# Kernel tuning notes

Hardware: AMD Instinct MI355X
Metric: run time of the kernel (lower is better)

Reference implementation:

```python
import jax, jax.numpy as jnp
import numpy as np

DIM = 1024
NUM_HEADS = 16
HEAD_DIM = DIM // NUM_HEADS
FF = 4 * DIM
B, T, S = 8, 512, 4096


def setup_inputs() -> dict:
    key = jax.random.key(0)
    ks = jax.random.split(key, 14)
    sc = 1.0 / np.sqrt(DIM)
    inp = {
        "x": jax.random.normal(ks[0], (B, T, DIM), jnp.float32),
        "inp": jax.random.normal(ks[1], (B, S, DIM), jnp.float32),
        # attention projections
        "Wq": jax.random.normal(ks[2], (DIM, DIM), jnp.float32) * sc,
        "bq": jnp.zeros((DIM,), jnp.float32),
        "Wk": jax.random.normal(ks[3], (DIM, DIM), jnp.float32) * sc,
        "bk": jnp.zeros((DIM,), jnp.float32),
        "Wv": jax.random.normal(ks[4], (DIM, DIM), jnp.float32) * sc,
        "bv": jnp.zeros((DIM,), jnp.float32),
        "Wo": jax.random.normal(ks[5], (DIM, DIM), jnp.float32) * sc,
        "bo": jnp.zeros((DIM,), jnp.float32),
        # MLP
        "W1": jax.random.normal(ks[6], (DIM, FF), jnp.float32) * sc,
        "b1": jnp.zeros((FF,), jnp.float32),
        "W2": jax.random.normal(ks[7], (FF, DIM), jnp.float32) * (1.0 / np.sqrt(FF)),
        "b2": jnp.zeros((DIM,), jnp.float32),
    }
    return inp


def _perceiver_layer(x, inp, Wq, bq, Wk, bk, Wv, bv, Wo, bo, W1, b1, W2, b2):
    b, t, _ = x.shape
    s = inp.shape[1]
    q = (x @ Wq + bq).reshape(b, t, NUM_HEADS, HEAD_DIM)
    k = (inp @ Wk + bk).reshape(b, s, NUM_HEADS, HEAD_DIM)
    v = (inp @ Wv + bv).reshape(b, s, NUM_HEADS, HEAD_DIM)
    # [b, h, t, s] score tensor (as in original code)
    attn = jnp.einsum('bthd,bshd->bhts', q, k)
    attn = jax.nn.softmax(attn / jnp.sqrt(jnp.float32(HEAD_DIM)), axis=-1)
    out = jnp.einsum('bhts,bshd->bthd', attn, v).reshape(b, t, DIM)
    attn_out = out @ Wo + bo
    x = x + attn_out
    h = jax.nn.gelu(x @ W1 + b1, approximate=True)  # flax nn.gelu default is tanh approx
    x = x + (h @ W2 + b2)
    return x


def reference(x, inp, Wq, bq, Wk, bk, Wv, bv, Wo, bo, W1, b1, W2, b2):
    return _perceiver_layer(x, inp, Wq, bq, Wk, bk, Wv, bv, Wo, bo, W1, b1, W2, b2)
```

## Files before the change

### kernel.cpp

```cpp
#include <hip/hip_runtime.h>
#include <hip/hip_bf16.h>

#define DIM 1024
#define NHEADS 16
#define HDIM 64
#define FF_ 4096
#define BB 8
#define TT 512
#define SS 4096

typedef __attribute__((ext_vector_type(8))) __bf16 bf16x8;
typedef __attribute__((ext_vector_type(4))) float f32x4;
typedef __attribute__((ext_vector_type(4))) unsigned short us4;

#define SWZ(r, b) ((b) ^ (((r) & 7) << 4))

typedef const __attribute__((address_space(1))) void gvoid_t;
typedef __attribute__((address_space(3))) void lvoid_t;

__device__ __forceinline__ void ldst16(const void* g, void* l) {
  __builtin_amdgcn_global_load_lds((gvoid_t*)g, (lvoid_t*)l, 16, 0, 0);
}

__device__ inline unsigned short f2bf(float f) {
  unsigned u = __float_as_uint(f);
  u += 0x7fff + ((u >> 16) & 1);
  return (unsigned short)(u >> 16);
}

__device__ __forceinline__ unsigned cvt_pk(float lo, float hi) {
  unsigned r;
  asm("v_cvt_pk_bf16_f32 %0, %1, %2" : "=v"(r) : "v"(lo), "v"(hi));
  return r;
}

__global__ void cvt_f32_bf16(const float* __restrict__ in,
                             unsigned short* __restrict__ out, int n4) {
  int i = blockIdx.x * blockDim.x + threadIdx.x;
  int stride = gridDim.x * blockDim.x;
  for (; i < n4; i += stride) {
    float4 v = ((const float4*)in)[i];
    uint2 w = {cvt_pk(v.x, v.y), cvt_pk(v.z, v.w)};
    ((uint2*)out)[i] = w;
  }
}

__global__ void transpose_f32_bf16(const float* __restrict__ in,
                                   unsigned short* __restrict__ out,
                                   int R, int C) {
  __shared__ float tile[32][33];
  int bc = blockIdx.x * 32, br = blockIdx.y * 32;
  int tx = threadIdx.x & 31, ty = threadIdx.x >> 5;
#pragma unroll
  for (int i = 0; i < 32; i += 8)
    tile[ty + i][tx] = in[(size_t)(br + ty + i) * C + bc + tx];
  __syncthreads();
#pragma unroll
  for (int i = 0; i < 32; i += 8)
    out[(size_t)(bc + ty + i) * R + br + tx] = f2bf(tile[tx][ty + i]);
}

__global__ void transpose_v(const unsigned short* __restrict__ in,
                            unsigned short* __restrict__ out) {
  __shared__ unsigned short tile[32][33];
  int b = blockIdx.z;
  const unsigned short* ib = in + (size_t)b * SS * 2048 + 1024;
  unsigned short* ob = out + (size_t)b * DIM * SS;
  int bc = blockIdx.x * 32;
  int br = blockIdx.y * 32;
  int tx = threadIdx.x & 31, ty = threadIdx.x >> 5;
#pragma unroll
  for (int i = 0; i < 32; i += 8)
    tile[ty + i][tx] = ib[(size_t)(br + ty + i) * 2048 + bc + tx];
  __syncthreads();
#pragma unroll
  for (int i = 0; i < 32; i += 8)
    ob[(size_t)(bc + ty + i) * SS + br + tx] = tile[tx][ty + i];
}

template <int EPI>
__global__ __launch_bounds__(256, 3)
void gemm_kernel(const unsigned short* __restrict__ A,
                 const unsigned short* __restrict__ Bt,
                 const float* __restrict__ bias,
                 const float* __restrict__ res,
                 void* __restrict__ Cp,
                 unsigned short* __restrict__ C2,
                 int M, int N, int K) {
  __shared__ char smem[32768];
  char* As = smem;
  char* Bs = smem + 16384;

  const int tid = threadIdx.x;
  const int lane = tid & 63;
  const int wave = tid >> 6;
  const int wm = wave >> 1, wn = wave & 1;

  const int flat = blockIdx.y * gridDim.x + blockIdx.x;
  const int cpx = (gridDim.x * gridDim.y) >> 3;
  const int swz = (flat & 7) * cpx + (flat >> 3);
  const int m0 = (swz / gridDim.x) * 128, n0 = (swz % gridDim.x) * 128;

  f32x4 acc[4][4];
#pragma unroll
  for (int i = 0; i < 4; ++i)
#pragma unroll
    for (int j = 0; j < 4; ++j) acc[i][j] = (f32x4){0.f, 0.f, 0.f, 0.f};

  for (int k0 = 0; k0 < K; k0 += 64) {
    __syncthreads();
#pragma unroll
    for (int i = 0; i < 4; ++i) {
      int ch = (wave * 4 + i) * 64 + lane;
      int r = ch >> 3, c8 = (ch & 7) ^ (r & 7);
      ldst16(A + (size_t)(m0 + r) * K + k0 + c8 * 8, As + (wave * 4 + i) * 1024);
      ldst16(Bt + (size_t)(n0 + r) * K + k0 + c8 * 8, Bs + (wave * 4 + i) * 1024);
    }
    __syncthreads();

#pragma unroll
    for (int kk = 0; kk < 2; ++kk) {
      bf16x8 a[4], b[4];
#pragma unroll
      for (int mi = 0; mi < 4; ++mi) {
        int r = wm * 64 + mi * 16 + (lane & 15);
        a[mi] = *(const bf16x8*)(As + r * 128 + SWZ(r, kk * 64 + (lane >> 4) * 16));
      }
#pragma unroll
      for (int ni = 0; ni < 4; ++ni) {
        int r = wn * 64 + ni * 16 + (lane & 15);
        b[ni] = *(const bf16x8*)(Bs + r * 128 + SWZ(r, kk * 64 + (lane >> 4) * 16));
      }
#pragma unroll
      for (int mi = 0; mi < 4; ++mi)
#pragma unroll
        for (int ni = 0; ni < 4; ++ni)
          acc[mi][ni] = __builtin_amdgcn_mfma_f32_16x16x32_bf16(b[ni], a[mi], acc[mi][ni], 0, 0, 0);
    }
  }

  const int q = lane & 15, g4 = (lane >> 4) * 4;
#pragma unroll
  for (int mi = 0; mi < 4; ++mi) {
    int row = m0 + wm * 64 + mi * 16 + q;
#pragma unroll
    for (int ni = 0; ni < 4; ++ni) {
      int colb = n0 + wn * 64 + ni * 16 + g4;
      float4 bv = *(const float4*)(bias + colb);
      f32x4 v = acc[mi][ni];
      float v0 = v[0] + bv.x, v1 = v[1] + bv.y, v2 = v[2] + bv.z, v3 = v[3] + bv.w;
      if (EPI == 0) {
        uint2 w = {cvt_pk(v0, v1), cvt_pk(v2, v3)};
        *(uint2*)((unsigned short*)Cp + (size_t)row * N + colb) = w;
      } else if (EPI == 1) {
        float o[4] = {v0, v1, v2, v3};
#pragma unroll
        for (int j = 0; j < 4; ++j) {
          float u = 0.7978845608028654f * (o[j] + 0.044715f * o[j] * o[j] * o[j]);
          float e = __expf(2.f * u);
          float th = 1.f - 2.f / (e + 1.f);
          o[j] = 0.5f * o[j] * (1.f + th);
        }
        uint2 w = {cvt_pk(o[0], o[1]), cvt_pk(o[2], o[3])};
        *(uint2*)((unsigned short*)Cp + (size_t)row * N + colb) = w;
      } else {
        float4 r4 = *(const float4*)(res + (size_t)row * N + colb);
        float o0 = v0 + r4.x, o1 = v1 + r4.y, o2 = v2 + r4.z, o3 = v3 + r4.w;
        float4 ov = {o0, o1, o2, o3};
        *(float4*)((float*)Cp + (size_t)row * N + colb) = ov;
        if (EPI == 3) {
          uint2 w = {cvt_pk(o0, o1), cvt_pk(o2, o3)};
          *(uint2*)(C2 + (size_t)row * N + colb) = w;
        }
      }
    }
  }
}

__global__ __launch_bounds__(512, 4)
void attn_kernel3(const unsigned short* __restrict__ Qb,
                  const unsigned short* __restrict__ KVb,
                  const unsigned short* __restrict__ Vt,
                  unsigned short* __restrict__ Ob) {
  __shared__ char smem[65536];

  const int tid = threadIdx.x, lane = tid & 63, wave = tid >> 6;
  const int bid = blockIdx.x;
  const int b = bid & 7, qt = (bid >> 3) & 3, h = bid >> 5;
  const int q0 = qt * 128;
  const int q = lane & 15, g = lane >> 4;

  const int rK = tid >> 3;
  const int cK = (tid & 7) ^ (rK & 7);
  char* const Pw = smem + 49152 + wave * 2048;

  const unsigned short* srcQ = Qb + ((size_t)b * TT + q0) * DIM + h * HDIM;
  const unsigned short* srcK = KVb + (size_t)b * SS * 2048 + h * HDIM;
  const unsigned short* srcV = Vt + ((size_t)b * DIM + h * HDIM) * SS;

  {
    int r = tid >> 3, c = (tid & 7) ^ (r & 7);
    ldst16(srcQ + (size_t)r * DIM + c * 8, smem + tid * 16);
    int ch = tid + 512;
    r = ch >> 3; c = (ch & 7) ^ (r & 7);
    ldst16(srcQ + (size_t)r * DIM + c * 8, smem + ch * 16);
  }
  ldst16(srcK + (size_t)rK * 2048 + cK * 8, smem + 16384 + tid * 16);
  ldst16(srcV + (size_t)rK * SS + cK * 8, smem + 32768 + tid * 16);
  __syncthreads();

  bf16x8 qf[2];
  {
    int r = wave * 16 + q;
    qf[0] = *(const bf16x8*)(smem + r * 128 + SWZ(r, g * 16));
    qf[1] = *(const bf16x8*)(smem + r * 128 + SWZ(r, 64 + g * 16));
  }

  f32x4 acc[4];
#pragma unroll
  for (int dt = 0; dt < 4; ++dt) acc[dt] = (f32x4){0.f, 0.f, 0.f, 0.f};
  float lsum = 0.f;
  const float CSC = 0.125f * 1.4426950408889634f;

  const int NT = SS / 64;
  for (int t = 0; t < NT; ++t) {
    char* Kc = smem + 16384 + (t & 1) * 8192;
    char* Vc = smem + 32768 + (t & 1) * 8192;
    if (t + 1 < NT) {
      char* Kn = smem + 16384 + ((t + 1) & 1) * 8192;
      char* Vn = smem + 32768 + ((t + 1) & 1) * 8192;
      ldst16(srcK + (size_t)((t + 1) * 64 + rK) * 2048 + cK * 8, Kn + tid * 16);
      ldst16(srcV + (size_t)rK * SS + (t + 1) * 64 + cK * 8, Vn + tid * 16);
    }

    f32x4 st[4];
#pragma unroll
    for (int si = 0; si < 4; ++si) st[si] = (f32x4){0.f, 0.f, 0.f, 0.f};
#pragma unroll
    for (int kk = 0; kk < 2; ++kk)
#pragma unroll
      for (int si = 0; si < 4; ++si) {
        int r = si * 16 + q;
        bf16x8 kf = *(const bf16x8*)(Kc + r * 128 + SWZ(r, kk * 64 + g * 16));
        st[si] = __builtin_amdgcn_mfma_f32_16x16x32_bf16(kf, qf[kk], st[si], 0, 0, 0);
      }

    float rs = 0.f;
#pragma unroll
    for (int si = 0; si < 4; ++si) {
      float p0 = __builtin_amdgcn_exp2f(st[si][0] * CSC);
      float p1 = __builtin_amdgcn_exp2f(st[si][1] * CSC);
      float p2 = __builtin_amdgcn_exp2f(st[si][2] * CSC);
      float p3 = __builtin_amdgcn_exp2f(st[si][3] * CSC);
      rs += (p0 + p1) + (p2 + p3);
      uint2 w = {cvt_pk(p0, p1), cvt_pk(p2, p3)};
      *(uint2*)(Pw + q * 128 + SWZ(q, si * 32 + g * 8)) = w;
    }
    lsum += rs;

#pragma unroll
    for (int kk = 0; kk < 2; ++kk) {
      bf16x8 pb = *(const bf16x8*)(Pw + q * 128 + SWZ(q, kk * 64 + g * 16));
#pragma unroll
      for (int dt = 0; dt < 4; ++dt) {
        int r = dt * 16 + q;
        bf16x8 va = *(const bf16x8*)(Vc + r * 128 + SWZ(r, kk * 64 + g * 16));
        acc[dt] = __builtin_amdgcn_mfma_f32_16x16x32_bf16(va, pb, acc[dt], 0, 0, 0);
      }
    }
    __syncthreads();
  }

  lsum += __shfl_xor(lsum, 16);
  lsum += __shfl_xor(lsum, 32);
  float inv = 1.0f / lsum;
#pragma unroll
  for (int dt = 0; dt < 4; ++dt) {
    f32x4 v = acc[dt];
    uint2 w = {cvt_pk(v[0] * inv, v[1] * inv), cvt_pk(v[2] * inv, v[3] * inv)};
    *(uint2*)(Pw + q * 128 + SWZ(q, dt * 32 + g * 8)) = w;
  }
  __builtin_amdgcn_s_waitcnt(0);
  int qr = lane >> 2, cb = (lane & 3) * 32;
  uint4 lo = *(const uint4*)(Pw + qr * 128 + SWZ(qr, cb));
  uint4 hi = *(const uint4*)(Pw + qr * 128 + SWZ(qr, cb + 16));
  size_t ob = ((size_t)b * TT + q0 + wave * 16 + qr) * DIM + h * HDIM + (lane & 3) * 16;
  *(uint4*)(Ob + ob) = lo;
  *(uint4*)(Ob + ob + 8) = hi;
}

extern "C" void kernel_launch(void* const* d_in, const int* in_sizes, int n_in,
                              void* d_out, int out_size, void* d_ws, size_t ws_size,
                              hipStream_t stream) {
  const float* x   = (const float*)d_in[0];
  const float* inp = (const float*)d_in[1];
  const float* Wq  = (const float*)d_in[2];
  const float* bq  = (const float*)d_in[3];
  const float* Wk  = (const float*)d_in[4];
  const float* bk  = (const float*)d_in[5];
  const float* Wv  = (const float*)d_in[6];
  const float* bv  = (const float*)d_in[7];
  const float* Wo  = (const float*)d_in[8];
  const float* bo  = (const float*)d_in[9];
  const float* W1  = (const float*)d_in[10];
  const float* b1  = (const float*)d_in[11];
  const float* W2  = (const float*)d_in[12];
  const float* b2  = (const float*)d_in[13];
  float* out = (float*)d_out;

  char* ws = (char*)d_ws;
  const size_t MB = 1024ull * 1024ull;
  unsigned short* Wqt  = (unsigned short*)(ws + 0 * MB);
  unsigned short* Wkt  = (unsigned short*)(ws + 2 * MB);
  unsigned short* Wvt  = (unsigned short*)(ws + 4 * MB);
  unsigned short* Wkvt = Wkt;
  unsigned short* Wot  = (unsigned short*)(ws + 6 * MB);
  unsigned short* W1t  = (unsigned short*)(ws + 8 * MB);
  unsigned short* W2t  = (unsigned short*)(ws + 16 * MB);
  float*          bkv  = (float*)(ws + 24 * MB);
  unsigned short* Qb   = (unsigned short*)(ws + 25 * MB);
  unsigned short* KVb  = (unsigned short*)(ws + 33 * MB);
  float*          x2   = (float*)(ws + 33 * MB);
  unsigned short* x2b  = (unsigned short*)(ws + 49 * MB);
  unsigned short* hb   = (unsigned short*)(ws + 57 * MB);
  unsigned short* inpb = (unsigned short*)(ws + 161 * MB);
  unsigned short* Vt   = (unsigned short*)(ws + 161 * MB);
  unsigned short* xb   = (unsigned short*)(ws + 225 * MB);
  unsigned short* Obf  = (unsigned short*)d_out;

  hipMemcpyAsync(bkv, bk, 1024 * sizeof(float), hipMemcpyDeviceToDevice, stream);
  hipMemcpyAsync(bkv + 1024, bv, 1024 * sizeof(float), hipMemcpyDeviceToDevice, stream);

  cvt_f32_bf16<<<2048, 256, 0, stream>>>(inp, inpb, BB * SS * DIM / 4);
  cvt_f32_bf16<<<1024, 256, 0, stream>>>(x, xb, BB * TT * DIM / 4);

  transpose_f32_bf16<<<dim3(32, 32), 256, 0, stream>>>(Wq, Wqt, 1024, 1024);
  transpose_f32_bf16<<<dim3(32, 32), 256, 0, stream>>>(Wk, Wkt, 1024, 1024);
  transpose_f32_bf16<<<dim3(32, 32), 256, 0, stream>>>(Wv, Wvt, 1024, 1024);
  transpose_f32_bf16<<<dim3(32, 32), 256, 0, stream>>>(Wo, Wot, 1024, 1024);
  transpose_f32_bf16<<<dim3(128, 32), 256, 0, stream>>>(W1, W1t, 1024, 4096);
  transpose_f32_bf16<<<dim3(32, 128), 256, 0, stream>>>(W2, W2t, 4096, 1024);

  gemm_kernel<0><<<dim3(8, 32), 256, 0, stream>>>(xb, Wqt, bq, nullptr, Qb, nullptr, BB * TT, DIM, DIM);
  gemm_kernel<0><<<dim3(16, 256), 256, 0, stream>>>(inpb, Wkvt, bkv, nullptr, KVb, nullptr, BB * SS, 2048, DIM);

  transpose_v<<<dim3(32, 128, 8), 256, 0, stream>>>(KVb, Vt);

  attn_kernel3<<<dim3(512), 512, 0, stream>>>(Qb, KVb, Vt, Obf);

  gemm_kernel<3><<<dim3(8, 32), 256, 0, stream>>>(Obf, Wot, bo, x, x2, x2b, BB * TT, DIM, DIM);
  gemm_kernel<1><<<dim3(32, 32), 256, 0, stream>>>(x2b, W1t, b1, nullptr, hb, nullptr, BB * TT, FF_, DIM);
  gemm_kernel<2><<<dim3(8, 32), 256, 0, stream>>>(hb, W2t, b2, x2, out, nullptr, BB * TT, DIM, FF_);
}
```

Before: 513.9 us.

## Add 256x256 GEMM kernel, fuse V transpose into KV projection epilogue

Adds a new 512-thread GEMM with 256x256 tiles, a multi-stage global-to-LDS pipeline, and a grouped block-index swizzle. It replaces the K/V projection and the W1 MLP GEMM. The K/V projection epilogue writes K into a separate buffer and writes V already transposed, which removes the standalone transpose_v kernel and its extra pass over memory. The risks are that the transposed V stores are scattered 2-byte writes with poor coalescing, and that 128KB of LDS per block limits occupancy.

```diff
diff --git a/kernel.cpp b/kernel.cpp
--- a/kernel.cpp
+++ b/kernel.cpp
@@ -58,24 +58,6 @@
 #pragma unroll
   for (int i = 0; i < 32; i += 8)
     out[(size_t)(bc + ty + i) * R + br + tx] = f2bf(tile[tx][ty + i]);
-}
-
-__global__ void transpose_v(const unsigned short* __restrict__ in,
-                            unsigned short* __restrict__ out) {
-  __shared__ unsigned short tile[32][33];
-  int b = blockIdx.z;
-  const unsigned short* ib = in + (size_t)b * SS * 2048 + 1024;
-  unsigned short* ob = out + (size_t)b * DIM * SS;
-  int bc = blockIdx.x * 32;
-  int br = blockIdx.y * 32;
-  int tx = threadIdx.x & 31, ty = threadIdx.x >> 5;
-#pragma unroll
-  for (int i = 0; i < 32; i += 8)
-    tile[ty + i][tx] = ib[(size_t)(br + ty + i) * 2048 + bc + tx];
-  __syncthreads();
-#pragma unroll
-  for (int i = 0; i < 32; i += 8)
-    ob[(size_t)(bc + ty + i) * SS + br + tx] = tile[tx][ty + i];
 }
 
 template <int EPI>
@@ -177,9 +159,149 @@
   }
 }
 
+template <int EPI>
+__global__ __launch_bounds__(512, 2)
+void gemm256(const unsigned short* __restrict__ A,
+             const unsigned short* __restrict__ Bt,
+             const float* __restrict__ bias,
+             void* __restrict__ Cp,
+             unsigned short* __restrict__ C2,
+             int M, int N, int K) {
+  __shared__ char smem[131072];
+
+  const int tid = threadIdx.x, lane = tid & 63, wave = tid >> 6;
+  const int q = lane & 15, g = lane >> 4;
+  const int wm = wave >> 2, wn = wave & 3;
+
+  const int flat = blockIdx.y * gridDim.x + blockIdx.x;
+  const int cpx = (gridDim.x * gridDim.y) >> 3;
+  const int swz = (flat & 7) * cpx + (flat >> 3);
+  const int m0 = (swz / gridDim.x) * 256, n0 = (swz % gridDim.x) * 256;
+
+  const unsigned short* Arow = A + (size_t)m0 * K;
+  const unsigned short* Brow = Bt + (size_t)n0 * K;
+
+  const int r0 = tid >> 3, c0 = ((tid & 7) ^ (r0 & 7)) * 8;
+  const int r1 = (tid + 512) >> 3, c1 = (((tid + 512) & 7) ^ (r1 & 7)) * 8;
+
+#define STA(buf, half, kt)                                                     \
+  { char* d = smem + (buf) * 32768 + (half) * 16384;                           \
+    const unsigned short* s = Arow + (size_t)((half) * 128) * K + (kt) * 64;   \
+    ldst16(s + (size_t)r0 * K + c0, d + tid * 16);                             \
+    ldst16(s + (size_t)r1 * K + c1, d + 8192 + tid * 16); }
+#define STB(buf, half, kt)                                                     \
+  { char* d = smem + 65536 + (buf) * 32768 + (half) * 16384;                   \
+    const unsigned short* s = Brow + (size_t)((half) * 128) * K + (kt) * 64;   \
+    ldst16(s + (size_t)r0 * K + c0, d + tid * 16);                             \
+    ldst16(s + (size_t)r1 * K + c1, d + 8192 + tid * 16); }
+
+  f32x4 acc[8][4];
+#pragma unroll
+  for (int i = 0; i < 8; ++i)
+#pragma unroll
+    for (int j = 0; j < 4; ++j) acc[i][j] = (f32x4){0.f, 0.f, 0.f, 0.f};
+
+  STA(0, 0, 0); STA(0, 1, 0); STB(0, 0, 0); STB(0, 1, 0);
+  STB(1, 0, 1); STB(1, 1, 1); STA(1, 0, 1);
+  asm volatile("s_waitcnt vmcnt(6)" ::: "memory");
+  __builtin_amdgcn_s_barrier();
+
+  const int NKT = K >> 6;
+  for (int kt = 0; kt < NKT; ++kt) {
+    const int cb = kt & 1, nb = cb ^ 1;
+    const char* Ab = smem + cb * 32768;
+    const char* Bb = smem + 65536 + cb * 32768;
+    bf16x8 bfr[4][2];
+
+#pragma unroll
+    for (int p = 0; p < 4; ++p) {
+      if (p == 0) { if (kt + 1 < NKT) STA(nb, 1, kt + 1); }
+      else if (p == 1) { if (kt + 2 < NKT) STB(cb, 0, kt + 2); }
+      else if (p == 2) { if (kt + 2 < NKT) STB(cb, 1, kt + 2); }
+      else            { if (kt + 2 < NKT) STA(cb, 0, kt + 2); }
+
+      bf16x8 af[2][2];
+#pragma unroll
+      for (int i = 0; i < 2; ++i)
+#pragma unroll
+        for (int kk = 0; kk < 2; ++kk) {
+          int r = wm * 128 + (2 * p + i) * 16 + q;
+          af[i][kk] = *(const bf16x8*)(Ab + r * 128 + SWZ(r, kk * 64 + g * 16));
+        }
+      if (p == 0) {
+#pragma unroll
+        for (int nr = 0; nr < 4; ++nr)
+#pragma unroll
+          for (int kk = 0; kk < 2; ++kk) {
+            int r = wn * 64 + nr * 16 + q;
+            bfr[nr][kk] = *(const bf16x8*)(Bb + r * 128 + SWZ(r, kk * 64 + g * 16));
+          }
+      }
+
+      __builtin_amdgcn_s_barrier();
+      asm volatile("s_waitcnt lgkmcnt(0)" ::: "memory");
+      __builtin_amdgcn_sched_barrier(0);
+      __builtin_amdgcn_s_setprio(1);
+#pragma unroll
+      for (int i = 0; i < 2; ++i)
+#pragma unroll
+        for (int nr = 0; nr < 4; ++nr)
+#pragma unroll
+          for (int kk = 0; kk < 2; ++kk)
+            acc[2 * p + i][nr] = __builtin_amdgcn_mfma_f32_16x16x32_bf16(
+                bfr[nr][kk], af[i][kk], acc[2 * p + i][nr], 0, 0, 0);
+      __builtin_amdgcn_s_setprio(0);
+
+      if (p == 1) asm volatile("s_waitcnt vmcnt(10)" ::: "memory");
+      if (p == 3) asm volatile("s_waitcnt vmcnt(8)" ::: "memory");
+      __builtin_amdgcn_s_barrier();
+    }
+  }
+
+  const int g4 = g * 4;
+#pragma unroll
+  for (int mr = 0; mr < 8; ++mr) {
+    int row = m0 + wm * 128 + mr * 16 + q;
+#pragma unroll
+    for (int nr = 0; nr < 4; ++nr) {
+      int colb = n0 + wn * 64 + nr * 16 + g4;
+      float4 bv = *(const float4*)(bias + colb);
+      f32x4 v = acc[mr][nr];
+      float v0 = v[0] + bv.x, v1 = v[1] + bv.y, v2 = v[2] + bv.z, v3 = v[3] + bv.w;
+      if (EPI == 1) {
+        float o[4] = {v0, v1, v2, v3};
+#pragma unroll
+        for (int j = 0; j < 4; ++j) {
+          float u = 0.7978845608028654f * (o[j] + 0.044715f * o[j] * o[j] * o[j]);
+          float e = __expf(2.f * u);
+          float th = 1.f - 2.f / (e + 1.f);
+          o[j] = 0.5f * o[j] * (1.f + th);
+        }
+        uint2 w = {cvt_pk(o[0], o[1]), cvt_pk(o[2], o[3])};
+        *(uint2*)((unsigned short*)Cp + (size_t)row * N + colb) = w;
+      } else {
+        if (n0 < 1024) {
+          uint2 w = {cvt_pk(v0, v1), cvt_pk(v2, v3)};
+          *(uint2*)((unsigned short*)Cp + (size_t)row * 1024 + colb) = w;
+        } else {
+          int b = row >> 12, s = row & 4095;
+          int d0 = colb - 1024;
+          unsigned short* vt = C2 + ((size_t)b * DIM + d0) * SS + s;
+          vt[0] = f2bf(v0);
+          vt[SS] = f2bf(v1);
+          vt[2 * SS] = f2bf(v2);
+          vt[3 * SS] = f2bf(v3);
+        }
+      }
+    }
+  }
+#undef STA
+#undef STB
+}
+
 __global__ __launch_bounds__(512, 4)
 void attn_kernel3(const unsigned short* __restrict__ Qb,
-                  const unsigned short* __restrict__ KVb,
+                  const unsigned short* __restrict__ Kb,
                   const unsigned short* __restrict__ Vt,
                   unsigned short* __restrict__ Ob) {
   __shared__ char smem[65536];
@@ -195,7 +317,7 @@
   char* const Pw = smem + 49152 + wave * 2048;
 
   const unsigned short* srcQ = Qb + ((size_t)b * TT + q0) * DIM + h * HDIM;
-  const unsigned short* srcK = KVb + (size_t)b * SS * 2048 + h * HDIM;
+  const unsigned short* srcK = Kb + (size_t)b * SS * DIM + h * HDIM;
   const unsigned short* srcV = Vt + ((size_t)b * DIM + h * HDIM) * SS;
 
   {
@@ -205,7 +327,7 @@
     r = ch >> 3; c = (ch & 7) ^ (r & 7);
     ldst16(srcQ + (size_t)r * DIM + c * 8, smem + ch * 16);
   }
-  ldst16(srcK + (size_t)rK * 2048 + cK * 8, smem + 16384 + tid * 16);
+  ldst16(srcK + (size_t)rK * DIM + cK * 8, smem + 16384 + tid * 16);
   ldst16(srcV + (size_t)rK * SS + cK * 8, smem + 32768 + tid * 16);
   __syncthreads();
 
@@ -229,7 +351,7 @@
     if (t + 1 < NT) {
       char* Kn = smem + 16384 + ((t + 1) & 1) * 8192;
       char* Vn = smem + 32768 + ((t + 1) & 1) * 8192;
-      ldst16(srcK + (size_t)((t + 1) * 64 + rK) * 2048 + cK * 8, Kn + tid * 16);
+      ldst16(srcK + (size_t)((t + 1) * 64 + rK) * DIM + cK * 8, Kn + tid * 16);
       ldst16(srcV + (size_t)rK * SS + (t + 1) * 64 + cK * 8, Vn + tid * 16);
     }
 
@@ -319,12 +441,12 @@
   unsigned short* W2t  = (unsigned short*)(ws + 16 * MB);
   float*          bkv  = (float*)(ws + 24 * MB);
   unsigned short* Qb   = (unsigned short*)(ws + 25 * MB);
-  unsigned short* KVb  = (unsigned short*)(ws + 33 * MB);
+  unsigned short* Kb   = (unsigned short*)(ws + 33 * MB);
   float*          x2   = (float*)(ws + 33 * MB);
   unsigned short* x2b  = (unsigned short*)(ws + 49 * MB);
   unsigned short* hb   = (unsigned short*)(ws + 57 * MB);
+  unsigned short* Vt   = (unsigned short*)(ws + 97 * MB);
   unsigned short* inpb = (unsigned short*)(ws + 161 * MB);
-  unsigned short* Vt   = (unsigned short*)(ws + 161 * MB);
   unsigned short* xb   = (unsigned short*)(ws + 225 * MB);
   unsigned short* Obf  = (unsigned short*)d_out;
 
@@ -342,13 +464,11 @@
   transpose_f32_bf16<<<dim3(32, 128), 256, 0, stream>>>(W2, W2t, 4096, 1024);
 
   gemm_kernel<0><<<dim3(8, 32), 256, 0, stream>>>(xb, Wqt, bq, nullptr, Qb, nullptr, BB * TT, DIM, DIM);
-  gemm_kernel<0><<<dim3(16, 256), 256, 0, stream>>>(inpb, Wkvt, bkv, nullptr, KVb, nullptr, BB * SS, 2048, DIM);
-
-  transpose_v<<<dim3(32, 128, 8), 256, 0, stream>>>(KVb, Vt);
-
-  attn_kernel3<<<dim3(512), 512, 0, stream>>>(Qb, KVb, Vt, Obf);
+  gemm256<2><<<dim3(8, 128), 512, 0, stream>>>(inpb, Wkvt, bkv, Kb, Vt, BB * SS, 2048, DIM);
+
+  attn_kernel3<<<dim3(512), 512, 0, stream>>>(Qb, Kb, Vt, Obf);
 
   gemm_kernel<3><<<dim3(8, 32), 256, 0, stream>>>(Obf, Wot, bo, x, x2, x2b, BB * TT, DIM, DIM);
-  gemm_kernel<1><<<dim3(32, 32), 256, 0, stream>>>(x2b, W1t, b1, nullptr, hb, nullptr, BB * TT, FF_, DIM);
+  gemm256<1><<<dim3(16, 16), 512, 0, stream>>>(x2b, W1t, b1, hb, nullptr, BB * TT, FF_, DIM);
   gemm_kernel<2><<<dim3(8, 32), 256, 0, stream>>>(hb, W2t, b2, x2, out, nullptr, BB * TT, DIM, FF_);
 }
```

Result: faster. 472.0 us (-8.2%).
